# Optimization experiments

Hardware: AMD Instinct MI355X
Metric: run time of the kernel (lower is better)

## Reference

```python
import jax, jax.numpy as jnp
import numpy as np

B, S, M = 128, 4096, 20
LOG_2PI = float(np.log(2.0 * np.pi))


def setup_inputs() -> dict:
    key = jax.random.key(0)
    k1, k2, k3, k4, k5 = jax.random.split(key, 5)
    xs = jax.random.normal(k1, (B, S, 5), dtype=jnp.float32)
    logits_pred = jax.random.normal(k2, (B, S, M), dtype=jnp.float32)
    mus_pred = jax.random.normal(k3, (B, S, M, 2), dtype=jnp.float32)
    # sigmas are Cholesky entries (l00, l10, l11); diagonal must be positive.
    sigmas_pred = jax.random.uniform(k4, (B, S, M, 3), dtype=jnp.float32) + 0.1
    pen_pred = jax.random.uniform(k5, (B, S, 3), dtype=jnp.float32)
    return {"xs": xs, "logits_pred": logits_pred, "mus_pred": mus_pred,
            "sigmas_pred": sigmas_pred, "pen_pred": pen_pred}


def reference(xs, logits_pred, mus_pred, sigmas_pred, pen_pred):
    # split stroke-5 format: (dx_abs, dy_abs) + 3 pen states
    position_true = xs[..., :2]          # [B,S,2]
    pen_true = xs[..., 2:]               # [B,S,3]

    # relative positions: roll by 1 along seq, first step prev = (0,0)
    position_prev = jnp.concatenate(
        [jnp.zeros_like(position_true[:, :1]), position_true[:, :-1]], axis=1)
    rel = position_true - position_prev  # [B,S,2]

    # closed-form 2D Gaussian log-density with lower-tri Cholesky
    # scale_tril entries (tril_indices(2,2) order): l00, l10, l11
    l00 = sigmas_pred[..., 0]            # [B,S,M]
    l10 = sigmas_pred[..., 1]
    l11 = sigmas_pred[..., 2]
    d = rel[:, :, None, :] - mus_pred    # [B,S,M,2]
    z0 = d[..., 0] / l00
    z1 = (d[..., 1] - l10 * z0) / l11
    comp_logp = (-0.5 * (z0 * z0 + z1 * z1)
                 - LOG_2PI - jnp.log(l00) - jnp.log(l11))  # [B,S,M]

    # mixture log-prob via logsumexp over components
    mix_logp = jax.nn.logsumexp(
        jax.nn.log_softmax(logits_pred, axis=-1) + comp_logp, axis=-1)  # [B,S]
    position_loss = -jnp.sum(mix_logp)

    # pen loss: faithful to source -> CrossEntropyLoss(input=pen_true, target=pen_pred)
    # (soft-target CE, mean reduction over B*S rows)
    logp = jax.nn.log_softmax(pen_true.reshape(-1, 3), axis=-1)
    pen_loss = jnp.mean(-jnp.sum(pen_pred.reshape(-1, 3) * logp, axis=-1))

    return position_loss + pen_loss
```

## Files before the change

kernel.cpp:

```cpp
#include <hip/hip_runtime.h>
#include <math.h>

#define BB 128
#define SS 4096
#define MM 20
#define NPOS (BB * SS)
#define BLOCK 256
#define POS_PER_BLOCK 256
#define NBLOCKS (NPOS / POS_PER_BLOCK)
#define ITERS (POS_PER_BLOCK / 8)

__device__ __forceinline__ float fast_rcp(float x) { return __builtin_amdgcn_rcpf(x); }

__global__ __launch_bounds__(BLOCK) void sketch_main(
    const float* __restrict__ xs,
    const float* __restrict__ logits,
    const float* __restrict__ mus,
    const float* __restrict__ sigmas,
    const float* __restrict__ pen_pred,
    float* __restrict__ partials)
{
    const float LOG_2PI = 1.8378770664093453f;
    const int lane = threadIdx.x & 63;
    const int wave = threadIdx.x >> 6;
    const int half = lane >> 5;
    const int j    = lane & 31;
    const int wavebase = blockIdx.x * POS_PER_BLOCK + wave * 64;

    float acc = 0.0f;

#pragma unroll 4
    for (int t = 0; t < ITERS; ++t) {
        const int p = wavebase + t * 2 + half;
        const int s = p & (SS - 1);

        const float* xp = xs + (size_t)p * 5;
        float px = xp[0], py = xp[1];
        float qx = 0.0f, qy = 0.0f;
        if (s != 0) { qx = xp[-5]; qy = xp[-4]; }
        float rx = px - qx, ry = py - qy;

        float lgj = -INFINITY, a = -INFINITY;
        if (j < MM) {
            const float* sb = sigmas + (size_t)p * 60 + j * 3;
            float l00 = sb[0], l10 = sb[1], l11 = sb[2];
            const float* mb = mus + (size_t)p * 40 + j * 2;
            float m0 = mb[0], m1 = mb[1];
            lgj = logits[(size_t)p * 20 + j];
            float z0 = (rx - m0) * fast_rcp(l00);
            float z1 = ((ry - m1) - l10 * z0) * fast_rcp(l11);
            a = lgj - 0.5f * (z0 * z0 + z1 * z1) - LOG_2PI - __logf(l00 * l11);
        }

        float mx_a = a, mx_l = lgj;
#pragma unroll
        for (int off = 16; off; off >>= 1) {
            mx_a = fmaxf(mx_a, __shfl_xor(mx_a, off, 32));
            mx_l = fmaxf(mx_l, __shfl_xor(mx_l, off, 32));
        }
        float ea = (j < MM) ? __expf(a - mx_a)   : 0.0f;
        float el = (j < MM) ? __expf(lgj - mx_l) : 0.0f;
#pragma unroll
        for (int off = 16; off; off >>= 1) {
            ea += __shfl_xor(ea, off, 32);
            el += __shfl_xor(el, off, 32);
        }
        float mix_logp = (mx_a + __logf(ea)) - (mx_l + __logf(el));

        float pt0 = xp[2], pt1 = xp[3], pt2 = xp[4];
        float pm = fmaxf(pt0, fmaxf(pt1, pt2));
        float lse3 = pm + __logf(__expf(pt0 - pm) + __expf(pt1 - pm) + __expf(pt2 - pm));
        const float* pp = pen_pred + (size_t)p * 3;
        float pen = -(pp[0] * (pt0 - lse3) + pp[1] * (pt1 - lse3) + pp[2] * (pt2 - lse3));

        float val = -mix_logp + pen * (1.0f / (float)NPOS);
        acc += (j == 0) ? val : 0.0f;
    }

#pragma unroll
    for (int off = 32; off > 0; off >>= 1) acc += __shfl_down(acc, off, 64);
    __shared__ float red[BLOCK / 64];
    if (lane == 0) red[wave] = acc;
    __syncthreads();
    if (threadIdx.x == 0)
        partials[blockIdx.x] = red[0] + red[1] + red[2] + red[3];
}

__global__ __launch_bounds__(BLOCK) void sketch_reduce(
    const float* __restrict__ partials, float* __restrict__ out)
{
    float v = 0.0f;
    for (int i = threadIdx.x; i < NBLOCKS; i += BLOCK) v += partials[i];
#pragma unroll
    for (int off = 32; off > 0; off >>= 1) v += __shfl_down(v, off, 64);
    __shared__ float red[BLOCK / 64];
    int lane = threadIdx.x & 63, wid = threadIdx.x >> 6;
    if (lane == 0) red[wid] = v;
    __syncthreads();
    if (threadIdx.x == 0)
        out[0] = red[0] + red[1] + red[2] + red[3];
}

extern "C" void kernel_launch(void* const* d_in, const int* in_sizes, int n_in,
                              void* d_out, int out_size, void* d_ws, size_t ws_size,
                              hipStream_t stream) {
    const float* xs       = (const float*)d_in[0];
    const float* logits   = (const float*)d_in[1];
    const float* mus      = (const float*)d_in[2];
    const float* sigmas   = (const float*)d_in[3];
    const float* pen_pred = (const float*)d_in[4];
    float* out = (float*)d_out;
    float* partials = (float*)d_ws;

    sketch_main<<<NBLOCKS, BLOCK, 0, stream>>>(xs, logits, mus, sigmas, pen_pred, partials);
    sketch_reduce<<<1, BLOCK, 0, stream>>>(partials, out);
}
```

Baseline: 313.4 us.

## Stage mixture params via double-buffered async LDS loads, 4 threads per position

Replaces the 32-lanes-per-position layout with 4 threads per position, each handling 5 mixture components. The sigmas, mus and logits for each 64-position chunk are staged into shared memory through global_load_lds, double-buffered across 16 chunks per block. This aims to turn the strided, partly idle per-lane global loads into fully coalesced 16-byte transfers and to overlap loading with compute. It also computes the logits normaliser as a plain sum of exponentials without max subtraction, which risks overflow for large logits. The larger shared-memory footprint and fewer blocks may limit occupancy.

```diff
diff --git a/kernel.cpp b/kernel.cpp
--- a/kernel.cpp
+++ b/kernel.cpp
@@ -6,11 +6,35 @@
 #define MM 20
 #define NPOS (BB * SS)
 #define BLOCK 256
-#define POS_PER_BLOCK 256
-#define NBLOCKS (NPOS / POS_PER_BLOCK)
-#define ITERS (POS_PER_BLOCK / 8)
+#define CHUNK 64
+#define CPB 16
+#define GRID (NPOS / (CHUNK * CPB))
+#define BUF_FLOATS (CHUNK * 120)
 
 __device__ __forceinline__ float fast_rcp(float x) { return __builtin_amdgcn_rcpf(x); }
+
+__device__ __forceinline__ void async_ld16(float* lds, const float* g) {
+    __builtin_amdgcn_global_load_lds(
+        (const __attribute__((address_space(1))) void*)g,
+        (__attribute__((address_space(3))) void*)lds, 16, 0, 0);
+}
+
+__device__ __forceinline__ void stage_chunk(
+    float* __restrict__ buf, const float* __restrict__ sg,
+    const float* __restrict__ mg, const float* __restrict__ lg, int tid)
+{
+#pragma unroll
+    for (int r = 0; r < 7; ++r) {
+        int i = tid + r * 256;
+        if (i < 960)       async_ld16(buf + i * 4, sg + (size_t)i * 4);
+        else if (i < 1600) async_ld16(buf + i * 4, mg + (size_t)(i - 960) * 4);
+        else               async_ld16(buf + i * 4, lg + (size_t)(i - 1600) * 4);
+    }
+    if (tid < 128) {
+        int i = 1792 + tid;
+        async_ld16(buf + i * 4, lg + (size_t)(i - 1600) * 4);
+    }
+}
 
 __global__ __launch_bounds__(BLOCK) void sketch_main(
     const float* __restrict__ xs,
@@ -21,79 +45,97 @@
     float* __restrict__ partials)
 {
     const float LOG_2PI = 1.8378770664093453f;
-    const int lane = threadIdx.x & 63;
-    const int wave = threadIdx.x >> 6;
-    const int half = lane >> 5;
-    const int j    = lane & 31;
-    const int wavebase = blockIdx.x * POS_PER_BLOCK + wave * 64;
+    __shared__ float buf[2][BUF_FLOATS];
+    __shared__ float red[BLOCK / 64];
+
+    const int tid  = threadIdx.x;
+    const int pos  = tid >> 2;
+    const int sub  = tid & 3;
+    const int lane = tid & 63;
+    const int block_base = blockIdx.x * (CHUNK * CPB);
 
     float acc = 0.0f;
 
-#pragma unroll 4
-    for (int t = 0; t < ITERS; ++t) {
-        const int p = wavebase + t * 2 + half;
-        const int s = p & (SS - 1);
+    stage_chunk(buf[0], sigmas + (size_t)block_base * 60,
+                mus + (size_t)block_base * 40,
+                logits + (size_t)block_base * 20, tid);
 
+    for (int k = 0; k < CPB; ++k) {
+        __syncthreads();
+
+        const int base = block_base + (k + 1) * CHUNK;
+        if (k + 1 < CPB)
+            stage_chunk(buf[(k + 1) & 1], sigmas + (size_t)base * 60,
+                        mus + (size_t)base * 40, logits + (size_t)base * 20, tid);
+
+        const float* b = buf[k & 1];
+        const int p = block_base + k * CHUNK + pos;
         const float* xp = xs + (size_t)p * 5;
-        float px = xp[0], py = xp[1];
-        float qx = 0.0f, qy = 0.0f;
-        if (s != 0) { qx = xp[-5]; qy = xp[-4]; }
-        float rx = px - qx, ry = py - qy;
 
-        float lgj = -INFINITY, a = -INFINITY;
-        if (j < MM) {
-            const float* sb = sigmas + (size_t)p * 60 + j * 3;
-            float l00 = sb[0], l10 = sb[1], l11 = sb[2];
-            const float* mb = mus + (size_t)p * 40 + j * 2;
-            float m0 = mb[0], m1 = mb[1];
-            lgj = logits[(size_t)p * 20 + j];
+        float rx = 0.0f, ry = 0.0f, penv = 0.0f;
+        if (sub == 0) {
+            rx = xp[0]; ry = xp[1];
+            if ((p & (SS - 1)) != 0) { rx -= xp[-5]; ry -= xp[-4]; }
+        } else if (sub == 1) {
+            float pt0 = xp[2], pt1 = xp[3], pt2 = xp[4];
+            float pm = fmaxf(pt0, fmaxf(pt1, pt2));
+            float l3 = pm + __logf(__expf(pt0 - pm) + __expf(pt1 - pm) + __expf(pt2 - pm));
+            const float* pp = pen_pred + (size_t)p * 3;
+            penv = -(pp[0] * (pt0 - l3) + pp[1] * (pt1 - l3) + pp[2] * (pt2 - l3));
+        }
+        rx = __shfl(rx, lane & ~3, 64);
+        ry = __shfl(ry, lane & ~3, 64);
+
+        const float* S  = b + pos * 60;
+        const float* Mu = b + CHUNK * 60 + pos * 40;
+        const float* Lg = b + CHUNK * 100 + pos * 20;
+
+        float av[5];
+        float sel = 0.0f;
+#pragma unroll
+        for (int c5 = 0; c5 < 5; ++c5) {
+            int c = sub * 5 + c5;
+            float l00 = S[c * 3], l10 = S[c * 3 + 1], l11 = S[c * 3 + 2];
+            float m0 = Mu[c * 2], m1 = Mu[c * 2 + 1];
+            float lgv = Lg[c];
             float z0 = (rx - m0) * fast_rcp(l00);
             float z1 = ((ry - m1) - l10 * z0) * fast_rcp(l11);
-            a = lgj - 0.5f * (z0 * z0 + z1 * z1) - LOG_2PI - __logf(l00 * l11);
+            av[c5] = lgv - 0.5f * (z0 * z0 + z1 * z1) - LOG_2PI - __logf(l00 * l11);
+            sel += __expf(lgv);
         }
+        float mx = fmaxf(fmaxf(fmaxf(av[0], av[1]), fmaxf(av[2], av[3])), av[4]);
+        float se = __expf(av[0]-mx) + __expf(av[1]-mx) + __expf(av[2]-mx)
+                 + __expf(av[3]-mx) + __expf(av[4]-mx);
 
-        float mx_a = a, mx_l = lgj;
 #pragma unroll
-        for (int off = 16; off; off >>= 1) {
-            mx_a = fmaxf(mx_a, __shfl_xor(mx_a, off, 32));
-            mx_l = fmaxf(mx_l, __shfl_xor(mx_l, off, 32));
+        for (int off = 1; off <= 2; off <<= 1) {
+            float omx = __shfl_xor(mx, off, 64);
+            float ose = __shfl_xor(se, off, 64);
+            float osl = __shfl_xor(sel, off, 64);
+            float nm = fmaxf(mx, omx);
+            se = se * __expf(mx - nm) + ose * __expf(omx - nm);
+            mx = nm;
+            sel += osl;
         }
-        float ea = (j < MM) ? __expf(a - mx_a)   : 0.0f;
-        float el = (j < MM) ? __expf(lgj - mx_l) : 0.0f;
-#pragma unroll
-        for (int off = 16; off; off >>= 1) {
-            ea += __shfl_xor(ea, off, 32);
-            el += __shfl_xor(el, off, 32);
-        }
-        float mix_logp = (mx_a + __logf(ea)) - (mx_l + __logf(el));
-
-        float pt0 = xp[2], pt1 = xp[3], pt2 = xp[4];
-        float pm = fmaxf(pt0, fmaxf(pt1, pt2));
-        float lse3 = pm + __logf(__expf(pt0 - pm) + __expf(pt1 - pm) + __expf(pt2 - pm));
-        const float* pp = pen_pred + (size_t)p * 3;
-        float pen = -(pp[0] * (pt0 - lse3) + pp[1] * (pt1 - lse3) + pp[2] * (pt2 - lse3));
-
-        float val = -mix_logp + pen * (1.0f / (float)NPOS);
-        acc += (j == 0) ? val : 0.0f;
+        if (sub == 0) acc -= (mx + __logf(se)) - __logf(sel);
+        acc += penv * (1.0f / (float)NPOS);
     }
 
 #pragma unroll
     for (int off = 32; off > 0; off >>= 1) acc += __shfl_down(acc, off, 64);
-    __shared__ float red[BLOCK / 64];
-    if (lane == 0) red[wave] = acc;
+    if (lane == 0) red[tid >> 6] = acc;
     __syncthreads();
-    if (threadIdx.x == 0)
-        partials[blockIdx.x] = red[0] + red[1] + red[2] + red[3];
+    if (tid == 0) partials[blockIdx.x] = red[0] + red[1] + red[2] + red[3];
 }
 
-__global__ __launch_bounds__(BLOCK) void sketch_reduce(
+__global__ __launch_bounds__(256) void sketch_reduce(
     const float* __restrict__ partials, float* __restrict__ out)
 {
     float v = 0.0f;
-    for (int i = threadIdx.x; i < NBLOCKS; i += BLOCK) v += partials[i];
+    for (int i = threadIdx.x; i < GRID; i += 256) v += partials[i];
 #pragma unroll
     for (int off = 32; off > 0; off >>= 1) v += __shfl_down(v, off, 64);
-    __shared__ float red[BLOCK / 64];
+    __shared__ float red[4];
     int lane = threadIdx.x & 63, wid = threadIdx.x >> 6;
     if (lane == 0) red[wid] = v;
     __syncthreads();
@@ -112,6 +154,6 @@
     float* out = (float*)d_out;
     float* partials = (float*)d_ws;
 
-    sketch_main<<<NBLOCKS, BLOCK, 0, stream>>>(xs, logits, mus, sigmas, pen_pred, partials);
-    sketch_reduce<<<1, BLOCK, 0, stream>>>(partials, out);
+    sketch_main<<<GRID, BLOCK, 0, stream>>>(xs, logits, mus, sigmas, pen_pred, partials);
+    sketch_reduce<<<1, 256, 0, stream>>>(partials, out);
 }
```

Result: faster. 286.4 us (-8.6%).
